# Kernel tuning notes

Measured on AMD Instinct MI355X. Metric: run time of the kernel, lower is better.

Reference implementation:

```python
import jax, jax.numpy as jnp
import numpy as np
from math import sqrt

D = 512        # output_dim (layer_dims[-1])
H = 4          # num_heads
ATN = D // H   # atn_dim = 128
BERT_D = 768
B = 32         # number of graph pairs
NP = 4096
NH = 4096


def setup_inputs() -> dict:
    key = jax.random.key(0)
    ks = jax.random.split(key, 20)
    inp = {
        'ctx_p': jax.random.normal(ks[0], (NP, D), jnp.float32),
        'ctx_h': jax.random.normal(ks[1], (NH, D), jnp.float32),
        'lhs_p': jax.random.normal(ks[2], (NP, BERT_D), jnp.float32),
        'lhs_h': jax.random.normal(ks[3], (NH, BERT_D), jnp.float32),
        'batch_p': jnp.sort(jax.random.randint(ks[4], (NP,), 0, B)).astype(jnp.int64),
        'batch_h': jnp.sort(jax.random.randint(ks[5], (NH,), 0, B)).astype(jnp.int64),
        # learned parameters (stored [in, out])
        'Wq': jax.random.normal(ks[6], (D, D), jnp.float32) * 0.02,
        'bq': jnp.zeros((D,), jnp.float32),
        'Wk': jax.random.normal(ks[7], (D, D), jnp.float32) * 0.02,
        'bk': jnp.zeros((D,), jnp.float32),
        'Wv': jax.random.normal(ks[8], (BERT_D, BERT_D), jnp.float32) * 0.02,
        'bv': jnp.zeros((BERT_D,), jnp.float32),
        'W1': jax.random.normal(ks[9], (D + BERT_D, 256), jnp.float32) * 0.02,
        'b1': jnp.zeros((256,), jnp.float32),
        'W2': jax.random.normal(ks[10], (256, 128), jnp.float32) * 0.02,
        'ln_g': jnp.ones((128,), jnp.float32),
        'ln_b': jnp.zeros((128,), jnp.float32),
        'Wc': jax.random.normal(ks[11], (128, 3), jnp.float32) * 0.02,
        'bc': jnp.zeros((3,), jnp.float32),
    }
    return inp


def reference(ctx_p, ctx_h, lhs_p, lhs_h, batch_p, batch_h,
              Wq, bq, Wk, bk, Wv, bv, W1, b1, W2, ln_g, ln_b, Wc, bc):
    # q/k projections; torch code does .view(-1, atn_dim, num_heads) -> head is fastest axis
    qs = (ctx_h @ Wq + bq).reshape(-1, ATN, H)          # [nh, atn, H]
    ks = (ctx_p @ Wk + bk).reshape(-1, ATN, H)          # [np, atn, H]
    vs = (lhs_p @ Wv + bv).reshape(-1, H, BERT_D // H)  # [np, H, 768/H]

    atn = jnp.einsum('ndh,mdh->nmh', qs, ks) / sqrt(ATN)  # [nh, np, H]
    # faithful to original: positions where batch ids MATCH are set to -1e10
    mask_same = batch_h[:, None] == batch_p[None, :]       # [nh, np]
    atn = jnp.where(mask_same[:, :, None], jnp.float32(-1e10), atn)
    atn = jax.nn.softmax(atn, axis=1)                      # softmax over premise words m

    attended = jnp.einsum('nmh,mhd->nhd', atn, vs).reshape(-1, BERT_D)  # [nh, 768]

    feats = jnp.concatenate([ctx_h, lhs_h - attended], axis=1)  # [nh, D+768]
    h1 = jax.nn.gelu(feats @ W1 + b1, approximate=False)
    h2 = h1 @ W2                                                # Linear no bias
    mu = h2.mean(axis=-1, keepdims=True)
    var = ((h2 - mu) ** 2).mean(axis=-1, keepdims=True)
    h2 = (h2 - mu) * jax.lax.rsqrt(var + 1e-5) * ln_g + ln_b    # LayerNorm(128)

    # global_mean_pool over batch_h
    pooled = jax.ops.segment_sum(h2, batch_h, num_segments=B)
    counts = jax.ops.segment_sum(jnp.ones((h2.shape[0], 1), h2.dtype), batch_h, num_segments=B)
    pooled = pooled / jnp.maximum(counts, 1.0)

    return pooled @ Wc + bc  # [B, 3]
```

## Files before the change

kernel.cpp:

```cpp
#include <hip/hip_runtime.h>
#include <hip/hip_bf16.h>
#include <math.h>

#define NP_N 4096
#define NH_N 4096
#define D_N 512
#define BERT_N 768
#define H_N 4
#define B_N 32

typedef __attribute__((ext_vector_type(8))) short short8;
typedef __attribute__((ext_vector_type(4))) float f32x4;
typedef __attribute__((ext_vector_type(4))) unsigned short ush4;
typedef unsigned short ushort_t;

__device__ __forceinline__ void gl_lds16(const void* g, void* l) {
    __builtin_amdgcn_global_load_lds((const __attribute__((address_space(1))) void*)g,
                                     (__attribute__((address_space(3))) void*)l, 16, 0, 0);
}
__device__ __forceinline__ unsigned short f2bu(float f) {
    __hip_bfloat16 b = __float2bfloat16(f);
    return *reinterpret_cast<unsigned short*>(&b);
}
__device__ __forceinline__ float b2f(unsigned short u) {
    union { unsigned int i; float f; } x; x.i = ((unsigned int)u) << 16; return x.f;
}
__device__ __forceinline__ unsigned int pkbf(float a, float b) {
    union { __hip_bfloat162 h; unsigned int u; } x;
    x.h.x = __float2bfloat16(a);
    x.h.y = __float2bfloat16(b);
    return x.u;
}

#define EW_BLOCKS 512
__global__ __launch_bounds__(256) void convert_all(
    const float* __restrict__ ctx_h, const float* __restrict__ ctx_p,
    const float* __restrict__ lhs_p,
    const float* __restrict__ Wq, const float* __restrict__ Wk,
    const float* __restrict__ Wv, const float* __restrict__ W1,
    const float* __restrict__ bq, const float* __restrict__ bk,
    ushort_t* __restrict__ ctxp_bf, ushort_t* __restrict__ lhsp_bf,
    ushort_t* __restrict__ feats,
    ushort_t* __restrict__ Wqt, ushort_t* __restrict__ Wkt,
    ushort_t* __restrict__ Wvt, ushort_t* __restrict__ W1t,
    float* __restrict__ bqp, float* __restrict__ bkp)
{
    const int bid = blockIdx.x, t = threadIdx.x;
    if (bid < EW_BLOCKS) {
        const long N0 = 524288, N1 = 1048576, TOT = 1835008;
        for (long i = (long)bid * 256 + t; i < TOT; i += (long)EW_BLOCKS * 256) {
            float4 v; ush4 o;
            if (i < N0) {
                long k = i;
                v = ((const float4*)ctx_h)[k];
                o[0] = f2bu(v.x); o[1] = f2bu(v.y); o[2] = f2bu(v.z); o[3] = f2bu(v.w);
                long n = k >> 7, c4 = k & 127;
                ((ush4*)feats)[n * 320 + c4] = o;
            } else if (i < N1) {
                long k = i - N0;
                v = ((const float4*)ctx_p)[k];
                o[0] = f2bu(v.x); o[1] = f2bu(v.y); o[2] = f2bu(v.z); o[3] = f2bu(v.w);
                ((ush4*)ctxp_bf)[k] = o;
            } else {
                long k = i - N1;
                v = ((const float4*)lhs_p)[k];
                o[0] = f2bu(v.x); o[1] = f2bu(v.y); o[2] = f2bu(v.z); o[3] = f2bu(v.w);
                ((ush4*)lhsp_bf)[k] = o;
            }
        }
        if (bid == 0) {
            for (int n = t; n < 512; n += 256) {
                int np = (n & 3) * 128 + (n >> 2);
                bqp[np] = bq[n];
                bkp[np] = bk[n];
            }
        }
        return;
    }
    int tb = bid - EW_BLOCKS;
    const float* src; ushort_t* dst; int K, N, tile, perm;
    if (tb < 64)       { src = Wq; dst = Wqt; K = 512;  N = 512; tile = tb;       perm = 1; }
    else if (tb < 128) { src = Wk; dst = Wkt; K = 512;  N = 512; tile = tb - 64;  perm = 1; }
    else if (tb < 272) { src = Wv; dst = Wvt; K = 768;  N = 768; tile = tb - 128; perm = 0; }
    else               { src = W1; dst = W1t; K = 1280; N = 256; tile = tb - 272; perm = 0; }
    int ntn = N >> 6;
    int k0 = (tile / ntn) * 64, n0 = (tile % ntn) * 64;
    __shared__ float tl[64][65];
#pragma unroll
    for (int i = 0; i < 16; i++) {
        int idx = t + i * 256; int r = idx >> 6, c = idx & 63;
        tl[r][c] = src[(size_t)(k0 + r) * N + n0 + c];
    }
    __syncthreads();
#pragma unroll
    for (int i = 0; i < 16; i++) {
        int idx = t + i * 256; int r = idx >> 6, c = idx & 63;
        int n = n0 + r;
        int nr = perm ? ((n & 3) * 128 + (n >> 2)) : n;
        dst[(size_t)nr * K + k0 + c] = f2bu(tl[c][r]);
    }
}

template<int TN, int BIAS_ROW, int GELU>
__global__ __launch_bounds__(256) void gemm2(
    const ushort_t* __restrict__ A, int lda, const ushort_t* __restrict__ Bt,
    const float* __restrict__ bias, ushort_t* __restrict__ C,
    int M, int N, int K)
{
    constexpr int NF = TN / 32;
    __shared__ ushort_t As[2][128 * 64];
    __shared__ ushort_t Bs[2][TN * 64];
    const int t = threadIdx.x, w = t >> 6, lane = t & 63;
    const int lq = lane & 15, g = lane >> 4;
    const int wm = w >> 1, wn = w & 1;
    const int n0 = blockIdx.x * TN, m0 = blockIdx.y * 128;
    const int nsteps = K >> 6;

    f32x4 acc[4][NF] = {};

    auto STAGE = [&](int buf, int k0) {
#pragma unroll
        for (int jj = 0; jj < 4; jj++) {
            int j = w * 4 + jj;
            int r = j * 8 + (lane >> 3);
            int c = (lane & 7) * 16;
            int cs = c ^ ((r & 7) << 4);
            gl_lds16((const char*)A + ((size_t)(m0 + r) * lda + k0) * 2 + cs,
                     (void*)&As[buf][j * 512]);
        }
#pragma unroll
        for (int jj = 0; jj < TN / 32; jj++) {
            int j = w * (TN / 32) + jj;
            int r = j * 8 + (lane >> 3);
            int c = (lane & 7) * 16;
            int cs = c ^ ((r & 7) << 4);
            gl_lds16((const char*)Bt + ((size_t)(n0 + r) * K + k0) * 2 + cs,
                     (void*)&Bs[buf][j * 512]);
        }
    };

    STAGE(0, 0);
    asm volatile("s_waitcnt vmcnt(0)" ::: "memory");
    __builtin_amdgcn_s_barrier();
    int cur = 0;
    for (int s = 0; s < nsteps; s++) {
        if (s + 1 < nsteps) STAGE(cur ^ 1, (s + 1) * 64);
        const char* Ab = (const char*)&As[cur][0];
        const char* Bb = (const char*)&Bs[cur][0];
        const int swz = (lq & 7) << 4;
        short8 af[4][2], bfr[NF][2];
#pragma unroll
        for (int mf = 0; mf < 4; mf++) {
            int r = wm * 64 + mf * 16 + lq;
#pragma unroll
            for (int ks = 0; ks < 2; ks++)
                af[mf][ks] = *(const short8*)(Ab + r * 128 + ((ks * 64 + g * 16) ^ swz));
        }
#pragma unroll
        for (int nf = 0; nf < NF; nf++) {
            int r = wn * (TN / 2) + nf * 16 + lq;
#pragma unroll
            for (int ks = 0; ks < 2; ks++)
                bfr[nf][ks] = *(const short8*)(Bb + r * 128 + ((ks * 64 + g * 16) ^ swz));
        }
        __builtin_amdgcn_s_setprio(1);
#pragma unroll
        for (int mf = 0; mf < 4; mf++)
#pragma unroll
            for (int nf = 0; nf < NF; nf++)
#pragma unroll
                for (int ks = 0; ks < 2; ks++)
                    acc[mf][nf] = __builtin_amdgcn_mfma_f32_16x16x32_bf16(
                        af[mf][ks], bfr[nf][ks], acc[mf][nf], 0, 0, 0);
        __builtin_amdgcn_s_setprio(0);
        asm volatile("s_waitcnt vmcnt(0)" ::: "memory");
        __builtin_amdgcn_s_barrier();
        cur ^= 1;
    }

#pragma unroll
    for (int mf = 0; mf < 4; mf++) {
#pragma unroll
        for (int nf = 0; nf < NF; nf++) {
            int ncol = n0 + wn * (TN / 2) + nf * 16 + lq;
            float bcol = BIAS_ROW ? 0.f : bias[ncol];
#pragma unroll
            for (int j = 0; j < 4; j++) {
                int mrow = m0 + wm * 64 + mf * 16 + 4 * g + j;
                float v = acc[mf][nf][j] + (BIAS_ROW ? bias[mrow] : bcol);
                if (GELU) v = 0.5f * v * (1.f + erff(v * 0.70710678118654752f));
                C[(size_t)mrow * N + ncol] = f2bu(v);
            }
        }
    }
}

__global__ __launch_bounds__(512, 2) void attn_mfma(
    const ushort_t* __restrict__ Qb,
    const ushort_t* __restrict__ Kb,
    const ushort_t* __restrict__ Vtb,
    const int* __restrict__ batch_h, const int* __restrict__ batch_p,
    ushort_t* __restrict__ Opart,
    float* __restrict__ ml)
{
    const int bid = blockIdx.x;
    const int h = (bid & 7) >> 1;
    const int s = bid & 1;
    const int n0 = (bid >> 3) * 128;

    __shared__ __align__(16) char smem[163840];

    const int t = threadIdx.x;
    const int w = t >> 6, o = w >> 2, wq = w & 3;
    const int lane = t & 63, lq = lane & 15, g = lane >> 4;
    const int lqm = (lq & 7) << 4;
    const float scl2 = 0.12754245006257576f;

    char* Kt0 = smem + (o * 2 + 0) * 16384;
    char* Kt1 = smem + (o * 2 + 1) * 16384;
    char* Vt0 = smem + 65536 + (o * 2 + 0) * 24576;
    char* Vt1 = smem + 65536 + (o * 2 + 1) * 24576;

    short8 qf[2][4];
    int bhq[2];
#pragma unroll
    for (int qg = 0; qg < 2; qg++) {
        const ushort_t* qrow = Qb + (size_t)(n0 + wq * 32 + qg * 16 + lq) * 512 + h * 128;
#pragma unroll
        for (int ks = 0; ks < 4; ks++)
            qf[qg][ks] = *(const short8*)(qrow + ks * 32 + g * 8);
        bhq[qg] = batch_h[n0 + wq * 32 + qg * 16 + lq];
    }
    const int bh_lo = batch_h[n0 + wq * 32];
    const int bh_hi = batch_h[n0 + wq * 32 + 31];

    f32x4 Ofr[2][12];
#pragma unroll
    for (int qg = 0; qg < 2; qg++)
#pragma unroll
        for (int nt = 0; nt < 12; nt++) Ofr[qg][nt] = (f32x4){0.f, 0.f, 0.f, 0.f};
    float m_run[2] = {-1e30f, -1e30f}, l_run[2] = {0.f, 0.f};

    const char* Kg = (const char*)Kb;
    const char* Vg = (const char*)Vtb;
    const int kb = s * 2048 + o * 1024;

    auto STAGE = [&](char* Kd, char* Vd, int m0k) {
#pragma unroll
        for (int jj = 0; jj < 4; jj++) {
            int j = wq * 4 + jj;
            int r = j * 4 + (lane >> 4);
            int c = (lane & 15) * 16;
            gl_lds16(Kg + (size_t)(m0k + r) * 1024 + h * 256 + (c ^ ((r & 7) << 4)),
                     Kd + j * 1024);
        }
#pragma unroll
        for (int jj = 0; jj < 6; jj++) {
            int j = wq * 6 + jj;
            int r = j * 8 + (lane >> 3);
            int c = (lane & 7) * 16;
            gl_lds16(Vg + ((size_t)(h * 192 + r) * 4096 + m0k) * 2 + (c ^ ((r & 7) << 4)),
                     Vd + j * 1024);
        }
    };

    STAGE(Kt0, Vt0, kb);
    asm volatile("s_waitcnt vmcnt(0)" ::: "memory");
    __builtin_amdgcn_s_barrier();
    int cur = 0;

    for (int tile = 0; tile < 16; tile++) {
        char* Kc = cur ? Kt1 : Kt0;
        char* Vc = cur ? Vt1 : Vt0;
        if (tile + 1 < 16) STAGE(cur ? Kt0 : Kt1, cur ? Vt0 : Vt1, kb + (tile + 1) * 64);

        const int ktb = kb + tile * 64;
        const int kt_lo = batch_p[ktb];
        const int kt_hi = batch_p[ktb + 63];
        const bool allmask = (kt_lo == kt_hi) && (kt_lo == bh_lo) && (bh_lo == bh_hi);
        const bool needmask = (kt_lo <= bh_hi) && (kt_hi >= bh_lo);

        if (!allmask) {
            f32x4 S[2][4];
#pragma unroll
            for (int qg = 0; qg < 2; qg++)
#pragma unroll
                for (int mt = 0; mt < 4; mt++) S[qg][mt] = (f32x4){0.f, 0.f, 0.f, 0.f};
            __builtin_amdgcn_s_setprio(1);
#pragma unroll
            for (int mt = 0; mt < 4; mt++) {
                const char* rbase = Kc + (mt * 16 + lq) * 256;
#pragma unroll
                for (int ks = 0; ks < 4; ks++) {
                    short8 kf = *(const short8*)(rbase + ((ks * 64 + g * 16) ^ lqm));
                    S[0][mt] = __builtin_amdgcn_mfma_f32_16x16x32_bf16(kf, qf[0][ks], S[0][mt], 0, 0, 0);
                    S[1][mt] = __builtin_amdgcn_mfma_f32_16x16x32_bf16(kf, qf[1][ks], S[1][mt], 0, 0, 0);
                }
            }
            __builtin_amdgcn_s_setprio(0);

            float mx[2];
            if (needmask) {
                int4 bp4[4];
#pragma unroll
                for (int mt = 0; mt < 4; mt++)
                    bp4[mt] = *(const int4*)&batch_p[ktb + mt * 16 + 4 * g];
#pragma unroll
                for (int qg = 0; qg < 2; qg++) {
                    float m = -1e30f;
#pragma unroll
                    for (int mt = 0; mt < 4; mt++) {
                        float v0 = (bp4[mt].x == bhq[qg]) ? -1e9f : S[qg][mt][0] * scl2;
                        float v1 = (bp4[mt].y == bhq[qg]) ? -1e9f : S[qg][mt][1] * scl2;
                        float v2 = (bp4[mt].z == bhq[qg]) ? -1e9f : S[qg][mt][2] * scl2;
                        float v3 = (bp4[mt].w == bhq[qg]) ? -1e9f : S[qg][mt][3] * scl2;
                        S[qg][mt][0] = v0; S[qg][mt][1] = v1; S[qg][mt][2] = v2; S[qg][mt][3] = v3;
                        m = fmaxf(m, fmaxf(fmaxf(v0, v1), fmaxf(v2, v3)));
                    }
                    m = fmaxf(m, __shfl_xor(m, 16));
                    m = fmaxf(m, __shfl_xor(m, 32));
                    mx[qg] = m;
                }
            } else {
#pragma unroll
                for (int qg = 0; qg < 2; qg++) {
                    float m = -1e30f;
#pragma unroll
                    for (int mt = 0; mt < 4; mt++) {
                        float v0 = S[qg][mt][0] * scl2;
                        float v1 = S[qg][mt][1] * scl2;
                        float v2 = S[qg][mt][2] * scl2;
                        float v3 = S[qg][mt][3] * scl2;
                        S[qg][mt][0] = v0; S[qg][mt][1] = v1; S[qg][mt][2] = v2; S[qg][mt][3] = v3;
                        m = fmaxf(m, fmaxf(fmaxf(v0, v1), fmaxf(v2, v3)));
                    }
                    m = fmaxf(m, __shfl_xor(m, 16));
                    m = fmaxf(m, __shfl_xor(m, 32));
                    mx[qg] = m;
                }
            }
            bool ng = __all((mx[0] <= m_run[0] + 8.f) && (mx[1] <= m_run[1] + 8.f));

            uint2 P2[2][4];
#pragma unroll
            for (int qg = 0; qg < 2; qg++) {
                float m_new = ng ? m_run[qg] : fmaxf(m_run[qg], mx[qg]);
                float rsum = 0.f;
#pragma unroll
                for (int mt = 0; mt < 4; mt++) {
                    float e0 = exp2f(S[qg][mt][0] - m_new);
                    float e1 = exp2f(S[qg][mt][1] - m_new);
                    float e2 = exp2f(S[qg][mt][2] - m_new);
                    float e3 = exp2f(S[qg][mt][3] - m_new);
                    rsum += (e0 + e1) + (e2 + e3);
                    P2[qg][mt].x = pkbf(e0, e1);
                    P2[qg][mt].y = pkbf(e2, e3);
                }
                rsum += __shfl_xor(rsum, 16);
                rsum += __shfl_xor(rsum, 32);
                if (ng) {
                    l_run[qg] += rsum;
                } else {
                    float f = exp2f(m_run[qg] - m_new);
                    l_run[qg] = l_run[qg] * f + rsum;
                    m_run[qg] = m_new;
                    float fr0 = __shfl(f, 4 * g + 0);
                    float fr1 = __shfl(f, 4 * g + 1);
                    float fr2 = __shfl(f, 4 * g + 2);
                    float fr3 = __shfl(f, 4 * g + 3);
#pragma unroll
                    for (int nt = 0; nt < 12; nt++) {
                        Ofr[qg][nt][0] *= fr0; Ofr[qg][nt][1] *= fr1;
                        Ofr[qg][nt][2] *= fr2; Ofr[qg][nt][3] *= fr3;
                    }
                }
            }

            __builtin_amdgcn_s_barrier();

            char* Pz = Kc + wq * 4096;
#pragma unroll
            for (int qg = 0; qg < 2; qg++)
#pragma unroll
                for (int mt = 0; mt < 4; mt++)
                    *(uint2*)(Pz + qg * 2048 + lq * 128 + ((mt * 32 + g * 8) ^ lqm)) = P2[qg][mt];

            __builtin_amdgcn_s_setprio(1);
#pragma unroll
            for (int ks = 0; ks < 2; ks++) {
                short8 pf0 = *(const short8*)(Pz + 0 * 2048 + lq * 128 + ((ks * 64 + g * 16) ^ lqm));
                short8 pf1 = *(const short8*)(Pz + 1 * 2048 + lq * 128 + ((ks * 64 + g * 16) ^ lqm));
#pragma unroll
                for (int nt = 0; nt < 12; nt++) {
                    short8 vf = *(const short8*)(Vc + (nt * 16 + lq) * 128 + ((ks * 64 + g * 16) ^ lqm));
                    Ofr[0][nt] = __builtin_amdgcn_mfma_f32_16x16x32_bf16(pf0, vf, Ofr[0][nt], 0, 0, 0);
                    Ofr[1][nt] = __builtin_amdgcn_mfma_f32_16x16x32_bf16(pf1, vf, Ofr[1][nt], 0, 0, 0);
                }
            }
            __builtin_amdgcn_s_setprio(0);
        } else {
            __builtin_amdgcn_s_barrier();
        }

        asm volatile("s_waitcnt vmcnt(0)" ::: "memory");
        __builtin_amdgcn_s_barrier();
        cur ^= 1;
    }

    const int tq = wq * 64 + lane;
    float* mOf = (float*)smem;
    float* mls = (float*)(smem + 98304);
    if (o == 1) {
#pragma unroll
        for (int qg = 0; qg < 2; qg++) {
#pragma unroll
            for (int nt = 0; nt < 12; nt++)
                *(f32x4*)(mOf + tq * 96 + qg * 48 + nt * 4) = Ofr[qg][nt];
            if (g == 0) {
                mls[(wq * 16 + lq) * 4 + qg * 2 + 0] = m_run[qg];
                mls[(wq * 16 + lq) * 4 + qg * 2 + 1] = l_run[qg];
            }
        }
    }
    __syncthreads();
    if (o == 0) {
        const size_t plane = (size_t)(s * 4 + h) * 4096;
#pragma unroll
        for (int qg = 0; qg < 2; qg++) {
            float m1 = mls[(wq * 16 + lq) * 4 + qg * 2 + 0];
            float l1 = mls[(wq * 16 + lq) * 4 + qg * 2 + 1];
            float m = fmaxf(m_run[qg], m1);
            float a0 = exp2f(m_run[qg] - m), a1 = exp2f(m1 - m);
            float l = l_run[qg] * a0 + l1 * a1;
            int qrow = n0 + wq * 32 + qg * 16;
            if (g == 0) {
                ml[(plane + qrow + lq) * 2 + 0] = m;
                ml[(plane + qrow + lq) * 2 + 1] = l;
            }
            float f0[4], f1[4];
#pragma unroll
            for (int j = 0; j < 4; j++) {
                f0[j] = __shfl(a0, 4 * g + j);
                f1[j] = __shfl(a1, 4 * g + j);
            }
#pragma unroll
            for (int nt = 0; nt < 12; nt++) {
                f32x4 o1 = *(f32x4*)(mOf + tq * 96 + qg * 48 + nt * 4);
#pragma unroll
                for (int j = 0; j < 4; j++) {
                    float val = Ofr[qg][nt][j] * f0[j] + o1[j] * f1[j];
                    Opart[(plane + qrow + 4 * g + j) * 192 + nt * 16 + lq] = f2bu(val);
                }
            }
        }
    }
}

__global__ __launch_bounds__(256) void combine_feats(
    const ushort_t* __restrict__ Opart, const float* __restrict__ ml,
    const float* __restrict__ lhs_h, ushort_t* __restrict__ feats)
{
    const int t = threadIdx.x;
#pragma unroll
    for (int i = 0; i < 4; i++) {
        int q = blockIdx.x * 4 + i;
#pragma unroll
        for (int it = 0; it < 3; it++) {
            int c = t + it * 256;
            int h = c / 192, vd = c - h * 192;
            size_t i0 = (size_t)h * 4096 + q;
            size_t i1 = (size_t)(4 + h) * 4096 + q;
            float m0 = ml[i0 * 2], l0 = ml[i0 * 2 + 1];
            float m1 = ml[i1 * 2], l1 = ml[i1 * 2 + 1];
            float m = fmaxf(m0, m1);
            float e0 = exp2f(m0 - m), e1 = exp2f(m1 - m);
            float linv = 1.f / (l0 * e0 + l1 * e1);
            float O = (b2f(Opart[i0 * 192 + vd]) * e0 + b2f(Opart[i1 * 192 + vd]) * e1) * linv;
            feats[(size_t)q * 1280 + 512 + c] = f2bu(lhs_h[(size_t)q * 768 + c] - O);
        }
    }
}

__global__ __launch_bounds__(256) void h2_ln(
    const ushort_t* __restrict__ h1, const float* __restrict__ W2,
    const float* __restrict__ ln_g, const float* __restrict__ ln_b,
    float* __restrict__ h2out)
{
    const int n0 = blockIdx.x * 8;
    const int t = threadIdx.x;
    __shared__ float h1s[8][256];
    __shared__ float h2s[8][128];

#pragma unroll
    for (int i = 0; i < 8; i++) {
        int idx = t + i * 256; int r = idx >> 8, c = idx & 255;
        h1s[r][c] = b2f(h1[(size_t)(n0 + r) * 256 + c]);
    }
    __syncthreads();

    {
        int o2 = t & 127, gq = t >> 7;
        float acc[4] = {};
        for (int k4 = 0; k4 < 64; k4++) {
            float w0 = W2[(size_t)(k4 * 4 + 0) * 128 + o2];
            float w1 = W2[(size_t)(k4 * 4 + 1) * 128 + o2];
            float w2 = W2[(size_t)(k4 * 4 + 2) * 128 + o2];
            float w3 = W2[(size_t)(k4 * 4 + 3) * 128 + o2];
#pragma unroll
            for (int q = 0; q < 4; q++) {
                float4 hh = *(const float4*)&h1s[gq * 4 + q][k4 * 4];
                acc[q] += hh.x * w0 + hh.y * w1 + hh.z * w2 + hh.w * w3;
            }
        }
#pragma unroll
        for (int q = 0; q < 4; q++) h2s[gq * 4 + q][o2] = acc[q];
    }
    __syncthreads();

    {
        int wv = t >> 6, lane = t & 63;
#pragma unroll
        for (int sx = 0; sx < 2; sx++) {
            int nd = wv * 2 + sx;
            float x0 = h2s[nd][lane], x1 = h2s[nd][lane + 64];
            float sum = x0 + x1;
#pragma unroll
            for (int off = 32; off; off >>= 1) sum += __shfl_xor(sum, off);
            float mu = sum * (1.f / 128.f);
            float d0 = x0 - mu, d1 = x1 - mu;
            float s2 = d0 * d0 + d1 * d1;
#pragma unroll
            for (int off = 32; off; off >>= 1) s2 += __shfl_xor(s2, off);
            float rstd = rsqrtf(s2 * (1.f / 128.f) + 1e-5f);
            size_t base = (size_t)(n0 + nd) * 128;
            h2out[base + lane]      = d0 * rstd * ln_g[lane] + ln_b[lane];
            h2out[base + lane + 64] = d1 * rstd * ln_g[lane + 64] + ln_b[lane + 64];
        }
    }
}

__global__ void ranges_kernel(const int* __restrict__ bh, int* __restrict__ lo,
                              int Nn, int Bn)
{
    int n = blockIdx.x * blockDim.x + threadIdx.x;
    if (n >= Nn) return;
    int b = bh[n];
    int prev = (n == 0) ? -1 : bh[n - 1];
    for (int bb = prev + 1; bb <= b; bb++) lo[bb] = n;
    if (n == Nn - 1) for (int bb = b + 1; bb <= Bn; bb++) lo[bb] = Nn;
}

__global__ __launch_bounds__(128) void pool_cls(
    const float* __restrict__ h2, const int* __restrict__ lo,
    const float* __restrict__ Wc, const float* __restrict__ bc,
    float* __restrict__ out)
{
    int b = blockIdx.x, t = threadIdx.x;
    int s = lo[b], e = lo[b + 1];
    float acc = 0.f;
    for (int n = s; n < e; n++) acc += h2[(size_t)n * 128 + t];
    float pooled = acc / fmaxf((float)(e - s), 1.f);
    __shared__ float red[128];
    for (int c = 0; c < 3; c++) {
        red[t] = pooled * Wc[t * 3 + c];
        __syncthreads();
        for (int off = 64; off > 0; off >>= 1) {
            if (t < off) red[t] += red[t + off];
            __syncthreads();
        }
        if (t == 0) out[b * 3 + c] = red[0] + bc[c];
        __syncthreads();
    }
}

extern "C" void kernel_launch(void* const* d_in, const int* in_sizes, int n_in,
                              void* d_out, int out_size, void* d_ws, size_t ws_size,
                              hipStream_t stream)
{
    const float* ctx_p  = (const float*)d_in[0];
    const float* ctx_h  = (const float*)d_in[1];
    const float* lhs_p  = (const float*)d_in[2];
    const float* lhs_h  = (const float*)d_in[3];
    const int*   batch_p = (const int*)d_in[4];
    const int*   batch_h = (const int*)d_in[5];
    const float* Wq = (const float*)d_in[6];
    const float* bq = (const float*)d_in[7];
    const float* Wk = (const float*)d_in[8];
    const float* bk = (const float*)d_in[9];
    const float* Wv = (const float*)d_in[10];
    const float* bv = (const float*)d_in[11];
    const float* W1 = (const float*)d_in[12];
    const float* b1 = (const float*)d_in[13];
    const float* W2 = (const float*)d_in[14];
    const float* ln_g = (const float*)d_in[15];
    const float* ln_b = (const float*)d_in[16];
    const float* Wc = (const float*)d_in[17];
    const float* bc = (const float*)d_in[18];
    float* out = (float*)d_out;

    ushort_t* u = (ushort_t*)d_ws;
    ushort_t* ctxp_bf = u;
    ushort_t* lhsp_bf = ctxp_bf + 2097152;
    ushort_t* Wqt  = lhsp_bf + 3145728;
    ushort_t* Wkt  = Wqt + 262144;
    ushort_t* Wvt  = Wkt + 262144;
    ushort_t* Opart = u;
    ushort_t* W1t  = Wvt + 589824;
    ushort_t* Qb   = W1t + 327680;
    ushort_t* Kb   = Qb + 2097152;
    ushort_t* Vtb  = Kb + 2097152;
    ushort_t* feats = Vtb + 3145728;
    ushort_t* h1   = feats + 5242880;
    float* ml  = (float*)(h1 + 1048576);
    float* h2  = ml + 65536;
    float* bqp = h2 + 524288;
    float* bkp = bqp + 512;
    int*   lo  = (int*)(bkp + 512);

    convert_all<<<864, 256, 0, stream>>>(
        ctx_h, ctx_p, lhs_p, Wq, Wk, Wv, W1, bq, bk,
        ctxp_bf, lhsp_bf, feats, Wqt, Wkt, Wvt, W1t, bqp, bkp);

    gemm2<128, 0, 0><<<dim3(4, 32), 256, 0, stream>>>(feats, 1280, Wqt, bqp, Qb, NH_N, 512, 512);
    gemm2<128, 0, 0><<<dim3(4, 32), 256, 0, stream>>>(ctxp_bf, 512, Wkt, bkp, Kb, NP_N, 512, 512);
    gemm2<128, 1, 0><<<dim3(32, 6), 256, 0, stream>>>(Wvt, 768, lhsp_bf, bv, Vtb, 768, NP_N, 768);

    attn_mfma<<<256, 512, 0, stream>>>(Qb, Kb, Vtb, batch_h, batch_p, Opart, ml);

    combine_feats<<<1024, 256, 0, stream>>>(Opart, ml, lhs_h, feats);

    gemm2<64, 0, 1><<<dim3(4, 32), 256, 0, stream>>>(feats, 1280, W1t, b1, h1, NH_N, 256, 1280);

    h2_ln<<<512, 256, 0, stream>>>(h1, W2, ln_g, ln_b, h2);
    ranges_kernel<<<16, 256, 0, stream>>>(batch_h, lo, NH_N, B_N);
    pool_cls<<<B_N, 128, 0, stream>>>(h2, lo, Wc, bc, out);
}
```

Before: 219.0 us.

## Fold softmax scale into Wq, shuffle-build P fragments, shrink GEMM tiles

Result: faster. 202.8 us (-7.4%).

```diff
diff --git a/kernel.cpp b/kernel.cpp
--- a/kernel.cpp
+++ b/kernel.cpp
@@ -8,10 +8,12 @@
 #define BERT_N 768
 #define H_N 4
 #define B_N 32
+#define SCL2 0.12754245006257576f
 
 typedef __attribute__((ext_vector_type(8))) short short8;
 typedef __attribute__((ext_vector_type(4))) float f32x4;
 typedef __attribute__((ext_vector_type(4))) unsigned short ush4;
+typedef __attribute__((ext_vector_type(4))) unsigned int uivec4;
 typedef unsigned short ushort_t;
 
 __device__ __forceinline__ void gl_lds16(const void* g, void* l) {
@@ -30,6 +32,24 @@
     x.h.x = __float2bfloat16(a);
     x.h.y = __float2bfloat16(b);
     return x.u;
+}
+__device__ __forceinline__ unsigned int sxor(unsigned int v, int m) {
+    return (unsigned int)__shfl_xor((int)v, m);
+}
+
+__device__ __forceinline__ short8 mkfrag(uint2 u, uint2 v, bool hi, bool godd) {
+    unsigned ux32 = sxor(u.x, 32), uy32 = sxor(u.y, 32);
+    unsigned vx32 = sxor(v.x, 32), vy32 = sxor(v.y, 32);
+    unsigned ax = hi ? vx32 : u.x, bx = hi ? v.x : ux32;
+    unsigned ay = hi ? vy32 : u.y, by = hi ? v.y : uy32;
+    unsigned sbx = sxor(bx, 16), sax = sxor(ax, 16);
+    unsigned sby = sxor(by, 16), say = sxor(ay, 16);
+    uivec4 w;
+    w.x = godd ? sbx : ax;
+    w.y = godd ? sby : ay;
+    w.z = godd ? bx : sax;
+    w.w = godd ? by : say;
+    return __builtin_bit_cast(short8, w);
 }
 
 #define EW_BLOCKS 512
@@ -71,18 +91,18 @@
         if (bid == 0) {
             for (int n = t; n < 512; n += 256) {
                 int np = (n & 3) * 128 + (n >> 2);
-                bqp[np] = bq[n];
+                bqp[np] = bq[n] * SCL2;
                 bkp[np] = bk[n];
             }
         }
         return;
     }
     int tb = bid - EW_BLOCKS;
-    const float* src; ushort_t* dst; int K, N, tile, perm;
-    if (tb < 64)       { src = Wq; dst = Wqt; K = 512;  N = 512; tile = tb;       perm = 1; }
-    else if (tb < 128) { src = Wk; dst = Wkt; K = 512;  N = 512; tile = tb - 64;  perm = 1; }
-    else if (tb < 272) { src = Wv; dst = Wvt; K = 768;  N = 768; tile = tb - 128; perm = 0; }
-    else               { src = W1; dst = W1t; K = 1280; N = 256; tile = tb - 272; perm = 0; }
+    const float* src; ushort_t* dst; int K, N, tile, perm; float wscl;
+    if (tb < 64)       { src = Wq; dst = Wqt; K = 512;  N = 512; tile = tb;       perm = 1; wscl = SCL2; }
+    else if (tb < 128) { src = Wk; dst = Wkt; K = 512;  N = 512; tile = tb - 64;  perm = 1; wscl = 1.f; }
+    else if (tb < 272) { src = Wv; dst = Wvt; K = 768;  N = 768; tile = tb - 128; perm = 0; wscl = 1.f; }
+    else               { src = W1; dst = W1t; K = 1280; N = 256; tile = tb - 272; perm = 0; wscl = 1.f; }
     int ntn = N >> 6;
     int k0 = (tile / ntn) * 64, n0 = (tile % ntn) * 64;
     __shared__ float tl[64][65];
@@ -97,31 +117,32 @@
         int idx = t + i * 256; int r = idx >> 6, c = idx & 63;
         int n = n0 + r;
         int nr = perm ? ((n & 3) * 128 + (n >> 2)) : n;
-        dst[(size_t)nr * K + k0 + c] = f2bu(tl[c][r]);
-    }
-}
-
-template<int TN, int BIAS_ROW, int GELU>
+        dst[(size_t)nr * K + k0 + c] = f2bu(tl[c][r] * wscl);
+    }
+}
+
+template<int TM, int TN, int BIAS_ROW, int GELU>
 __global__ __launch_bounds__(256) void gemm2(
     const ushort_t* __restrict__ A, int lda, const ushort_t* __restrict__ Bt,
     const float* __restrict__ bias, ushort_t* __restrict__ C,
     int M, int N, int K)
 {
-    constexpr int NF = TN / 32;
-    __shared__ ushort_t As[2][128 * 64];
+    constexpr int MF = TM / 32, NF = TN / 32;
+    constexpr int AI = TM / 32, BI = TN / 32;
+    __shared__ ushort_t As[2][TM * 64];
     __shared__ ushort_t Bs[2][TN * 64];
     const int t = threadIdx.x, w = t >> 6, lane = t & 63;
     const int lq = lane & 15, g = lane >> 4;
     const int wm = w >> 1, wn = w & 1;
-    const int n0 = blockIdx.x * TN, m0 = blockIdx.y * 128;
+    const int n0 = blockIdx.x * TN, m0 = blockIdx.y * TM;
     const int nsteps = K >> 6;
 
-    f32x4 acc[4][NF] = {};
+    f32x4 acc[MF][NF] = {};
 
     auto STAGE = [&](int buf, int k0) {
 #pragma unroll
-        for (int jj = 0; jj < 4; jj++) {
-            int j = w * 4 + jj;
+        for (int jj = 0; jj < AI; jj++) {
+            int j = w * AI + jj;
             int r = j * 8 + (lane >> 3);
             int c = (lane & 7) * 16;
             int cs = c ^ ((r & 7) << 4);
@@ -129,8 +150,8 @@
                      (void*)&As[buf][j * 512]);
         }
 #pragma unroll
-        for (int jj = 0; jj < TN / 32; jj++) {
-            int j = w * (TN / 32) + jj;
+        for (int jj = 0; jj < BI; jj++) {
+            int j = w * BI + jj;
             int r = j * 8 + (lane >> 3);
             int c = (lane & 7) * 16;
             int cs = c ^ ((r & 7) << 4);
@@ -148,10 +169,10 @@
         const char* Ab = (const char*)&As[cur][0];
         const char* Bb = (const char*)&Bs[cur][0];
         const int swz = (lq & 7) << 4;
-        short8 af[4][2], bfr[NF][2];
-#pragma unroll
-        for (int mf = 0; mf < 4; mf++) {
-            int r = wm * 64 + mf * 16 + lq;
+        short8 af[MF][2], bfr[NF][2];
+#pragma unroll
+        for (int mf = 0; mf < MF; mf++) {
+            int r = wm * (TM / 2) + mf * 16 + lq;
 #pragma unroll
             for (int ks = 0; ks < 2; ks++)
                 af[mf][ks] = *(const short8*)(Ab + r * 128 + ((ks * 64 + g * 16) ^ swz));
@@ -165,7 +186,7 @@
         }
         __builtin_amdgcn_s_setprio(1);
 #pragma unroll
-        for (int mf = 0; mf < 4; mf++)
+        for (int mf = 0; mf < MF; mf++)
 #pragma unroll
             for (int nf = 0; nf < NF; nf++)
 #pragma unroll
@@ -179,14 +200,14 @@
     }
 
 #pragma unroll
-    for (int mf = 0; mf < 4; mf++) {
+    for (int mf = 0; mf < MF; mf++) {
 #pragma unroll
         for (int nf = 0; nf < NF; nf++) {
             int ncol = n0 + wn * (TN / 2) + nf * 16 + lq;
             float bcol = BIAS_ROW ? 0.f : bias[ncol];
 #pragma unroll
             for (int j = 0; j < 4; j++) {
-                int mrow = m0 + wm * 64 + mf * 16 + 4 * g + j;
+                int mrow = m0 + wm * (TM / 2) + mf * 16 + 4 * g + j;
                 float v = acc[mf][nf][j] + (BIAS_ROW ? bias[mrow] : bcol);
                 if (GELU) v = 0.5f * v * (1.f + erff(v * 0.70710678118654752f));
                 C[(size_t)mrow * N + ncol] = f2bu(v);
@@ -214,7 +235,8 @@
     const int w = t >> 6, o = w >> 2, wq = w & 3;
     const int lane = t & 63, lq = lane & 15, g = lane >> 4;
     const int lqm = (lq & 7) << 4;
-    const float scl2 = 0.12754245006257576f;
+    const bool hi = lane >= 32;
+    const bool godd = (lane & 16) != 0;
 
     char* Kt0 = smem + (o * 2 + 0) * 16384;
     char* Kt1 = smem + (o * 2 + 1) * 16384;
@@ -231,8 +253,6 @@
             qf[qg][ks] = *(const short8*)(qrow + ks * 32 + g * 8);
         bhq[qg] = batch_h[n0 + wq * 32 + qg * 16 + lq];
     }
-    const int bh_lo = batch_h[n0 + wq * 32];
-    const int bh_hi = batch_h[n0 + wq * 32 + 31];
 
     f32x4 Ofr[2][12];
 #pragma unroll
@@ -272,139 +292,113 @@
     for (int tile = 0; tile < 16; tile++) {
         char* Kc = cur ? Kt1 : Kt0;
         char* Vc = cur ? Vt1 : Vt0;
+        const int ktb = kb + tile * 64;
+
+        int4 bp4[4];
+#pragma unroll
+        for (int mt = 0; mt < 4; mt++)
+            bp4[mt] = *(const int4*)&batch_p[ktb + mt * 16 + 4 * g];
+
         if (tile + 1 < 16) STAGE(cur ? Kt0 : Kt1, cur ? Vt0 : Vt1, kb + (tile + 1) * 64);
 
-        const int ktb = kb + tile * 64;
-        const int kt_lo = batch_p[ktb];
-        const int kt_hi = batch_p[ktb + 63];
-        const bool allmask = (kt_lo == kt_hi) && (kt_lo == bh_lo) && (bh_lo == bh_hi);
-        const bool needmask = (kt_lo <= bh_hi) && (kt_hi >= bh_lo);
-
-        if (!allmask) {
-            f32x4 S[2][4];
-#pragma unroll
-            for (int qg = 0; qg < 2; qg++)
-#pragma unroll
-                for (int mt = 0; mt < 4; mt++) S[qg][mt] = (f32x4){0.f, 0.f, 0.f, 0.f};
+        f32x4 S[2][4];
+#pragma unroll
+        for (int qg = 0; qg < 2; qg++)
+#pragma unroll
+            for (int mt = 0; mt < 4; mt++) S[qg][mt] = (f32x4){0.f, 0.f, 0.f, 0.f};
+        __builtin_amdgcn_s_setprio(1);
+#pragma unroll
+        for (int mt = 0; mt < 4; mt++) {
+            const char* rbase = Kc + (mt * 16 + lq) * 256;
+#pragma unroll
+            for (int ks = 0; ks < 4; ks++) {
+                short8 kf = *(const short8*)(rbase + ((ks * 64 + g * 16) ^ lqm));
+                S[0][mt] = __builtin_amdgcn_mfma_f32_16x16x32_bf16(kf, qf[0][ks], S[0][mt], 0, 0, 0);
+                S[1][mt] = __builtin_amdgcn_mfma_f32_16x16x32_bf16(kf, qf[1][ks], S[1][mt], 0, 0, 0);
+            }
+        }
+        __builtin_amdgcn_s_setprio(0);
+
+        float pmax[2];
+#pragma unroll
+        for (int qg = 0; qg < 2; qg++) {
+            float m = -1e30f;
+#pragma unroll
+            for (int mt = 0; mt < 4; mt++) {
+                float v0 = (bp4[mt].x == bhq[qg]) ? -1e9f : S[qg][mt][0];
+                float v1 = (bp4[mt].y == bhq[qg]) ? -1e9f : S[qg][mt][1];
+                float v2 = (bp4[mt].z == bhq[qg]) ? -1e9f : S[qg][mt][2];
+                float v3 = (bp4[mt].w == bhq[qg]) ? -1e9f : S[qg][mt][3];
+                S[qg][mt][0] = v0; S[qg][mt][1] = v1; S[qg][mt][2] = v2; S[qg][mt][3] = v3;
+                m = fmaxf(m, fmaxf(fmaxf(v0, v1), fmaxf(v2, v3)));
+            }
+            pmax[qg] = m;
+        }
+        bool ng = __all((pmax[0] <= m_run[0] + 8.f) && (pmax[1] <= m_run[1] + 8.f));
+        if (!ng) {
+#pragma unroll
+            for (int qg = 0; qg < 2; qg++) {
+                float mq = fmaxf(pmax[qg], m_run[qg]);
+                mq = fmaxf(mq, __shfl_xor(mq, 16));
+                mq = fmaxf(mq, __shfl_xor(mq, 32));
+                float f = exp2f(m_run[qg] - mq);
+                m_run[qg] = mq;
+                l_run[qg] *= f;
+                float fr0 = __shfl(f, 4 * g + 0);
+                float fr1 = __shfl(f, 4 * g + 1);
+                float fr2 = __shfl(f, 4 * g + 2);
+                float fr3 = __shfl(f, 4 * g + 3);
+#pragma unroll
+                for (int nt = 0; nt < 12; nt++) {
+                    Ofr[qg][nt][0] *= fr0; Ofr[qg][nt][1] *= fr1;
+                    Ofr[qg][nt][2] *= fr2; Ofr[qg][nt][3] *= fr3;
+                }
+            }
+        }
+
+        uint2 P2[2][4];
+#pragma unroll
+        for (int qg = 0; qg < 2; qg++) {
+            float lsum = 0.f;
+#pragma unroll
+            for (int mt = 0; mt < 4; mt++) {
+                float e0 = exp2f(S[qg][mt][0] - m_run[qg]);
+                float e1 = exp2f(S[qg][mt][1] - m_run[qg]);
+                float e2 = exp2f(S[qg][mt][2] - m_run[qg]);
+                float e3 = exp2f(S[qg][mt][3] - m_run[qg]);
+                lsum += (e0 + e1) + (e2 + e3);
+                P2[qg][mt].x = pkbf(e0, e1);
+                P2[qg][mt].y = pkbf(e2, e3);
+            }
+            l_run[qg] += lsum;
+        }
+
+#pragma unroll
+        for (int ks = 0; ks < 2; ks++) {
+            short8 pf0 = mkfrag(P2[0][2 * ks], P2[0][2 * ks + 1], hi, godd);
+            short8 pf1 = mkfrag(P2[1][2 * ks], P2[1][2 * ks + 1], hi, godd);
             __builtin_amdgcn_s_setprio(1);
 #pragma unroll
-            for (int mt = 0; mt < 4; mt++) {
-                const char* rbase = Kc + (mt * 16 + lq) * 256;
-#pragma unroll
-                for (int ks = 0; ks < 4; ks++) {
-                    short8 kf = *(const short8*)(rbase + ((ks * 64 + g * 16) ^ lqm));
-                    S[0][mt] = __builtin_amdgcn_mfma_f32_16x16x32_bf16(kf, qf[0][ks], S[0][mt], 0, 0, 0);
-                    S[1][mt] = __builtin_amdgcn_mfma_f32_16x16x32_bf16(kf, qf[1][ks], S[1][mt], 0, 0, 0);
-                }
+            for (int nt = 0; nt < 12; nt++) {
+                short8 vf = *(const short8*)(Vc + (nt * 16 + lq) * 128 + ((ks * 64 + g * 16) ^ lqm));
+                Ofr[0][nt] = __builtin_amdgcn_mfma_f32_16x16x32_bf16(pf0, vf, Ofr[0][nt], 0, 0, 0);
+                Ofr[1][nt] = __builtin_amdgcn_mfma_f32_16x16x32_bf16(pf1, vf, Ofr[1][nt], 0, 0, 0);
             }
             __builtin_amdgcn_s_setprio(0);
-
-            float mx[2];
-            if (needmask) {
-                int4 bp4[4];
-#pragma unroll
-                for (int mt = 0; mt < 4; mt++)
-                    bp4[mt] = *(const int4*)&batch_p[ktb + mt * 16 + 4 * g];
-#pragma unroll
-                for (int qg = 0; qg < 2; qg++) {
-                    float m = -1e30f;
-#pragma unroll
-                    for (int mt = 0; mt < 4; mt++) {
-                        float v0 = (bp4[mt].x == bhq[qg]) ? -1e9f : S[qg][mt][0] * scl2;
-                        float v1 = (bp4[mt].y == bhq[qg]) ? -1e9f : S[qg][mt][1] * scl2;
-                        float v2 = (bp4[mt].z == bhq[qg]) ? -1e9f : S[qg][mt][2] * scl2;
-                        float v3 = (bp4[mt].w == bhq[qg]) ? -1e9f : S[qg][mt][3] * scl2;
-                        S[qg][mt][0] = v0; S[qg][mt][1] = v1; S[qg][mt][2] = v2; S[qg][mt][3] = v3;
-                        m = fmaxf(m, fmaxf(fmaxf(v0, v1), fmaxf(v2, v3)));
-                    }
-                    m = fmaxf(m, __shfl_xor(m, 16));
-                    m = fmaxf(m, __shfl_xor(m, 32));
-                    mx[qg] = m;
-                }
-            } else {
-#pragma unroll
-                for (int qg = 0; qg < 2; qg++) {
-                    float m = -1e30f;
-#pragma unroll
-                    for (int mt = 0; mt < 4; mt++) {
-                        float v0 = S[qg][mt][0] * scl2;
-                        float v1 = S[qg][mt][1] * scl2;
-                        float v2 = S[qg][mt][2] * scl2;
-                        float v3 = S[qg][mt][3] * scl2;
-                        S[qg][mt][0] = v0; S[qg][mt][1] = v1; S[qg][mt][2] = v2; S[qg][mt][3] = v3;
-                        m = fmaxf(m, fmaxf(fmaxf(v0, v1), fmaxf(v2, v3)));
-                    }
-                    m = fmaxf(m, __shfl_xor(m, 16));
-                    m = fmaxf(m, __shfl_xor(m, 32));
-                    mx[qg] = m;
-                }
-            }
-            bool ng = __all((mx[0] <= m_run[0] + 8.f) && (mx[1] <= m_run[1] + 8.f));
-
-            uint2 P2[2][4];
-#pragma unroll
-            for (int qg = 0; qg < 2; qg++) {
-                float m_new = ng ? m_run[qg] : fmaxf(m_run[qg], mx[qg]);
-                float rsum = 0.f;
-#pragma unroll
-                for (int mt = 0; mt < 4; mt++) {
-                    float e0 = exp2f(S[qg][mt][0] - m_new);
-                    float e1 = exp2f(S[qg][mt][1] - m_new);
-                    float e2 = exp2f(S[qg][mt][2] - m_new);
-                    float e3 = exp2f(S[qg][mt][3] - m_new);
-                    rsum += (e0 + e1) + (e2 + e3);
-                    P2[qg][mt].x = pkbf(e0, e1);
-                    P2[qg][mt].y = pkbf(e2, e3);
-                }
-                rsum += __shfl_xor(rsum, 16);
-                rsum += __shfl_xor(rsum, 32);
-                if (ng) {
-                    l_run[qg] += rsum;
-                } else {
-                    float f = exp2f(m_run[qg] - m_new);
-                    l_run[qg] = l_run[qg] * f + rsum;
-                    m_run[qg] = m_new;
-                    float fr0 = __shfl(f, 4 * g + 0);
-                    float fr1 = __shfl(f, 4 * g + 1);
-                    float fr2 = __shfl(f, 4 * g + 2);
-                    float fr3 = __shfl(f, 4 * g + 3);
-#pragma unroll
-                    for (int nt = 0; nt < 12; nt++) {
-                        Ofr[qg][nt][0] *= fr0; Ofr[qg][nt][1] *= fr1;
-                        Ofr[qg][nt][2] *= fr2; Ofr[qg][nt][3] *= fr3;
-                    }
-                }
-            }
-
-            __builtin_amdgcn_s_barrier();
-
-            char* Pz = Kc + wq * 4096;
-#pragma unroll
-            for (int qg = 0; qg < 2; qg++)
-#pragma unroll
-                for (int mt = 0; mt < 4; mt++)
-                    *(uint2*)(Pz + qg * 2048 + lq * 128 + ((mt * 32 + g * 8) ^ lqm)) = P2[qg][mt];
-
-            __builtin_amdgcn_s_setprio(1);
-#pragma unroll
-            for (int ks = 0; ks < 2; ks++) {
-                short8 pf0 = *(const short8*)(Pz + 0 * 2048 + lq * 128 + ((ks * 64 + g * 16) ^ lqm));
-                short8 pf1 = *(const short8*)(Pz + 1 * 2048 + lq * 128 + ((ks * 64 + g * 16) ^ lqm));
-#pragma unroll
-                for (int nt = 0; nt < 12; nt++) {
-                    short8 vf = *(const short8*)(Vc + (nt * 16 + lq) * 128 + ((ks * 64 + g * 16) ^ lqm));
-                    Ofr[0][nt] = __builtin_amdgcn_mfma_f32_16x16x32_bf16(pf0, vf, Ofr[0][nt], 0, 0, 0);
-                    Ofr[1][nt] = __builtin_amdgcn_mfma_f32_16x16x32_bf16(pf1, vf, Ofr[1][nt], 0, 0, 0);
-                }
-            }
-            __builtin_amdgcn_s_setprio(0);
-        } else {
-            __builtin_amdgcn_s_barrier();
         }
 
         asm volatile("s_waitcnt vmcnt(0)" ::: "memory");
         __builtin_amdgcn_s_barrier();
         cur ^= 1;
+    }
+
+    float lt[2];
+#pragma unroll
+    for (int qg = 0; qg < 2; qg++) {
+        float l = l_run[qg];
+        l += __shfl_xor(l, 16);
+        l += __shfl_xor(l, 32);
+        lt[qg] = l;
     }
 
     const int tq = wq * 64 + lane;
@@ -418,7 +412,7 @@
                 *(f32x4*)(mOf + tq * 96 + qg * 48 + nt * 4) = Ofr[qg][nt];
             if (g == 0) {
                 mls[(wq * 16 + lq) * 4 + qg * 2 + 0] = m_run[qg];
-                mls[(wq * 16 + lq) * 4 + qg * 2 + 1] = l_run[qg];
+                mls[(wq * 16 + lq) * 4 + qg * 2 + 1] = lt[qg];
             }
         }
     }
@@ -431,7 +425,7 @@
             float l1 = mls[(wq * 16 + lq) * 4 + qg * 2 + 1];
             float m = fmaxf(m_run[qg], m1);
             float a0 = exp2f(m_run[qg] - m), a1 = exp2f(m1 - m);
-            float l = l_run[qg] * a0 + l1 * a1;
+            float l = lt[qg] * a0 + l1 * a1;
             int qrow = n0 + wq * 32 + qg * 16;
             if (g == 0) {
                 ml[(plane + qrow + lq) * 2 + 0] = m;
@@ -621,15 +615,15 @@
         ctx_h, ctx_p, lhs_p, Wq, Wk, Wv, W1, bq, bk,
         ctxp_bf, lhsp_bf, feats, Wqt, Wkt, Wvt, W1t, bqp, bkp);
 
-    gemm2<128, 0, 0><<<dim3(4, 32), 256, 0, stream>>>(feats, 1280, Wqt, bqp, Qb, NH_N, 512, 512);
-    gemm2<128, 0, 0><<<dim3(4, 32), 256, 0, stream>>>(ctxp_bf, 512, Wkt, bkp, Kb, NP_N, 512, 512);
-    gemm2<128, 1, 0><<<dim3(32, 6), 256, 0, stream>>>(Wvt, 768, lhsp_bf, bv, Vtb, 768, NP_N, 768);
+    gemm2<128, 64, 0, 0><<<dim3(8, 32), 256, 0, stream>>>(feats, 1280, Wqt, bqp, Qb, NH_N, 512, 512);
+    gemm2<128, 64, 0, 0><<<dim3(8, 32), 256, 0, stream>>>(ctxp_bf, 512, Wkt, bkp, Kb, NP_N, 512, 512);
+    gemm2<128, 64, 1, 0><<<dim3(64, 6), 256, 0, stream>>>(Wvt, 768, lhsp_bf, bv, Vtb, 768, NP_N, 768);
 
     attn_mfma<<<256, 512, 0, stream>>>(Qb, Kb, Vtb, batch_h, batch_p, Opart, ml);
 
     combine_feats<<<1024, 256, 0, stream>>>(Opart, ml, lhs_h, feats);
 
-    gemm2<64, 0, 1><<<dim3(4, 32), 256, 0, stream>>>(feats, 1280, W1t, b1, h1, NH_N, 256, 1280);
+    gemm2<64, 64, 0, 1><<<dim3(4, 64), 256, 0, stream>>>(feats, 1280, W1t, b1, h1, NH_N, 256, 1280);
 
     h2_ln<<<512, 256, 0, stream>>>(h1, W2, ln_g, ln_b, h2);
     ranges_kernel<<<16, 256, 0, stream>>>(batch_h, lo, NH_N, B_N);
```
